# Kernel tuning notes

Measured on AMD Instinct MI355X. Metric: run time of the kernel, lower is better.

## Reference

```python
import jax, jax.numpy as jnp
import jax.scipy.linalg as jsl
import numpy as np

B, T, C = 2, 4096, 1024
HK = HV = 8           # linear_num_key_heads == linear_num_value_heads
DK = DV = 128         # linear_key_head_dim / linear_value_head_dim
CHUNK = 64
CONV_K = 4
KEY_DIM = HK * DK
VAL_DIM = HV * DV
CONV_DIM = 2 * KEY_DIM + VAL_DIM
EPS = 1e-6


def setup_inputs() -> dict:
    key = jax.random.key(0)
    ks = jax.random.split(key, 8)
    s = 0.02
    x = jax.random.normal(ks[0], (B, T, C), jnp.float32)
    W_qkvz = jax.random.normal(ks[1], (C, 2 * KEY_DIM + 2 * VAL_DIM), jnp.float32) * s
    W_ba = jax.random.normal(ks[2], (C, 2 * HV), jnp.float32) * s
    conv_w = jax.random.normal(ks[3], (CONV_DIM, 1, CONV_K), jnp.float32) * 0.3  # depthwise (O,1,K)
    dt_bias = jnp.ones((HV,), jnp.float32)
    A_log = jnp.log(jax.random.uniform(ks[4], (HV,), jnp.float32, 0.5, 8.0))
    norm_weight = jnp.ones((DV,), jnp.float32)
    W_out = jax.random.normal(ks[5], (VAL_DIM, C), jnp.float32) * s
    return {"x": x, "W_qkvz": W_qkvz, "W_ba": W_ba, "conv_w": conv_w,
            "dt_bias": dt_bias, "A_log": A_log, "norm_weight": norm_weight, "W_out": W_out}


def _l2norm(x, eps=EPS):
    return x * jax.lax.rsqrt(jnp.sum(x * x, -1, keepdims=True) + eps)


def _chunk_gated_delta_rule(q, k, v, g, beta, chunk=CHUNK):
    # q,k: (B,T,H,DK); v: (B,T,H,DV); g,beta: (B,T,H)
    q = _l2norm(q)
    k = _l2norm(k)
    tr = lambda x: jnp.swapaxes(x, 1, 2).astype(jnp.float32)  # -> (B,H,T,...)
    q, k, v, g, beta = tr(q), tr(k), tr(v), tr(g), tr(beta)
    b, h, t, dk = k.shape
    dv = v.shape[-1]
    n = t // chunk  # T divisible by chunk (pad_size == 0)
    q = q * (dk ** -0.5)
    v_beta = v * beta[..., None]
    k_beta = k * beta[..., None]
    rs = lambda x: x.reshape(b, h, n, chunk, x.shape[-1])
    q, k, v_beta, k_beta = rs(q), rs(k), rs(v_beta), rs(k_beta)
    g = jnp.cumsum(g.reshape(b, h, n, chunk), axis=-1)
    # decay_mask[..., i, j] = exp(g_i - g_j) for j <= i, else 0
    decay = jnp.tril(jnp.exp(jnp.tril(g[..., :, None] - g[..., None, :])))
    # forward substitution == unit-lower-triangular solve: (I + tri)^{-1}
    tri = jnp.tril(jnp.einsum('bhnck,bhndk->bhncd', k_beta, k) * decay, -1)
    eye = jnp.eye(chunk, dtype=jnp.float32)
    Tm = jsl.solve_triangular(eye + tri, jnp.broadcast_to(eye, tri.shape), lower=True)
    v_new = Tm @ v_beta                                   # (B,H,N,C,DV)
    k_cum = Tm @ (k_beta * jnp.exp(g)[..., None])         # (B,H,N,C,DK)
    keep_low = jnp.tril(jnp.ones((chunk, chunk), bool))

    def step(S, inp):
        q_i, k_i, v_i, kc_i, g_i, dm_i = inp              # (B,H,C,*)
        attn = jnp.where(keep_low, (q_i @ jnp.swapaxes(k_i, -1, -2)) * dm_i, 0.0)
        v_n = v_i - kc_i @ S
        out = (q_i * jnp.exp(g_i)[..., None]) @ S + attn @ v_n
        g_last = g_i[..., -1]
        S = S * jnp.exp(g_last)[..., None, None] + jnp.einsum(
            'bhck,bhcv->bhkv', k_i * jnp.exp(g_last[..., None] - g_i)[..., None], v_n)
        return S, out

    mv = lambda x: jnp.moveaxis(x, 2, 0)                  # chunk axis to front
    S0 = jnp.zeros((b, h, dk, dv), jnp.float32)
    S, outs = jax.lax.scan(step, S0, (mv(q), mv(k), mv(v_new), mv(k_cum), mv(g), mv(decay)))
    out = jnp.moveaxis(outs, 0, 2).reshape(b, h, t, dv)
    return jnp.swapaxes(out, 1, 2), S                     # (B,T,H,DV), (B,H,DK,DV)


def reference(x, W_qkvz, W_ba, conv_w, dt_bias, A_log, norm_weight, W_out):
    Bx, Tx, Cx = x.shape
    ratio = HV // HK
    qkvz = (x @ W_qkvz).reshape(Bx, Tx, HK, 2 * DK + 2 * ratio * DV)
    q, k, v, z = jnp.split(qkvz, [DK, 2 * DK, 2 * DK + ratio * DV], axis=3)
    v = v.reshape(Bx, Tx, HV, DV)
    z = z.reshape(Bx, Tx, HV, DV)
    ba = (x @ W_ba).reshape(Bx, Tx, HK, 2 * ratio)
    b_, a_ = jnp.split(ba, [ratio], axis=3)
    b_ = b_.reshape(Bx, Tx, HV)
    a_ = a_.reshape(Bx, Tx, HV)
    mixed = jnp.concatenate([q.reshape(Bx, Tx, -1), k.reshape(Bx, Tx, -1),
                             v.reshape(Bx, Tx, -1)], axis=-1)
    # causal depthwise conv1d (left pad K-1, take first T)
    xc = jnp.swapaxes(mixed, 1, 2)                        # (B, CONV_DIM, T)
    conv = jax.lax.conv_general_dilated(xc, conv_w, (1,), [(CONV_K - 1, 0)],
                                        dimension_numbers=('NCH', 'OIH', 'NCH'),
                                        feature_group_count=CONV_DIM)
    conv = jnp.swapaxes(jax.nn.silu(conv), 1, 2)          # (B,T,CONV_DIM)
    qc, kc, vc = jnp.split(conv, [KEY_DIM, 2 * KEY_DIM], axis=-1)
    qc = qc.reshape(Bx, Tx, HK, DK)
    kc = kc.reshape(Bx, Tx, HK, DK)
    vc = vc.reshape(Bx, Tx, HV, DV)
    if ratio > 1:
        qc = jnp.repeat(qc, ratio, axis=2)
        kc = jnp.repeat(kc, ratio, axis=2)
    beta = jax.nn.sigmoid(b_)
    g = -jnp.exp(A_log) * jax.nn.softplus(a_ + dt_bias)
    core, _ = _chunk_gated_delta_rule(qc, kc, vc, g, beta)
    # GatedRMSNorm over head_v_dim, gated by silu(z)
    h = core.astype(jnp.float32)
    var = jnp.mean(h * h, -1, keepdims=True)
    h = norm_weight * (h * jax.lax.rsqrt(var + EPS))
    h = h * jax.nn.silu(z.astype(jnp.float32))
    return h.reshape(Bx, Tx, VAL_DIM) @ W_out
```

## Files before the change

kernel.cpp:

```cpp
#include <hip/hip_runtime.h>
#include <cstddef>

#define Bx 2
#define Tn 4096
#define Hh 8

typedef unsigned short u16;
typedef unsigned int u32;
typedef __attribute__((ext_vector_type(8))) short short8;
typedef __attribute__((ext_vector_type(4))) float f32x4;

__device__ __forceinline__ float bf2f(u16 u) {
  u32 x = ((u32)u) << 16;
  return __uint_as_float(x);
}
__device__ __forceinline__ u16 f2bf(float f) {
  u32 x = __float_as_uint(f);
  u32 lsb = (x >> 16) & 1;
  x += 0x7fffu + lsb;
  return (u16)(x >> 16);
}
__device__ __forceinline__ u32 pack2(float a, float b) {
  return (u32)f2bf(a) | ((u32)f2bf(b) << 16);
}
__device__ __forceinline__ short8 cvt8(float4 f0, float4 f1) {
  uint4 p;
  p.x = pack2(f0.x, f0.y);
  p.y = pack2(f0.z, f0.w);
  p.z = pack2(f1.x, f1.y);
  p.w = pack2(f1.z, f1.w);
  return *(short8*)&p;
}
__device__ __forceinline__ void async16(u16* lds, const u16* g) {
  __builtin_amdgcn_global_load_lds((const __attribute__((address_space(1))) void*)g,
                                   (__attribute__((address_space(3))) void*)lds, 16, 0, 0);
}

__global__ __launch_bounds__(256) void conv_bf16(const float* __restrict__ X,
                                                 u16* __restrict__ Xb) {
  int i = (blockIdx.x * 256 + threadIdx.x) * 8;
  float4 v0 = *(const float4*)&X[i];
  float4 v1 = *(const float4*)&X[i + 4];
  uint4 pv;
  pv.x = pack2(v0.x, v0.y);
  pv.y = pack2(v0.z, v0.w);
  pv.z = pack2(v1.x, v1.y);
  pv.w = pack2(v1.z, v1.w);
  *(uint4*)&Xb[i] = pv;
}

__global__ __launch_bounds__(256) void transpose_bf16(const float* __restrict__ W,
                                                      u16* __restrict__ WT,
                                                      int K, int N) {
  __shared__ float tile[64][68];
  int nb = blockIdx.x, kb = blockIdx.y;
  int tid = threadIdx.x;
  int r = tid >> 4, c4 = (tid & 15) * 4;
#pragma unroll
  for (int p = 0; p < 4; p++) {
    int k = kb * 64 + p * 16 + r;
    float4 v = *(const float4*)&W[(size_t)k * N + nb * 64 + c4];
    tile[p * 16 + r][c4] = v.x;
    tile[p * 16 + r][c4 + 1] = v.y;
    tile[p * 16 + r][c4 + 2] = v.z;
    tile[p * 16 + r][c4 + 3] = v.w;
  }
  __syncthreads();
  int rn = tid >> 2, ck = (tid & 3) * 16;
#pragma unroll
  for (int s = 0; s < 2; s++) {
    int k0 = ck + s * 8;
    uint4 pv;
    pv.x = pack2(tile[k0 + 0][rn], tile[k0 + 1][rn]);
    pv.y = pack2(tile[k0 + 2][rn], tile[k0 + 3][rn]);
    pv.z = pack2(tile[k0 + 4][rn], tile[k0 + 5][rn]);
    pv.w = pack2(tile[k0 + 6][rn], tile[k0 + 7][rn]);
    *(uint4*)&WT[(size_t)(nb * 64 + rn) * K + kb * 64 + k0] = pv;
  }
}

__global__ __launch_bounds__(512, 1) void gemm_qkvz(const u16* __restrict__ A,
                                                    const u16* __restrict__ Bt,
                                                    u16* __restrict__ O1,
                                                    u16* __restrict__ O2) {
  const int K = 1024;
  extern __shared__ __align__(16) u16 gl[];
  int lin = blockIdx.x;
  int sl = (lin & 7) * 64 + (lin >> 3);
  int bm = sl & 31;
  int bn = sl >> 5;
  int tid = threadIdx.x;
  int wid = tid >> 6, lane = tid & 63;
  int wm = wid >> 2, wn = wid & 3;
  int m_lane = lane & 15, kgrp = lane >> 4, m7 = m_lane & 7;

  f32x4 acc[8][4];
#pragma unroll
  for (int i = 0; i < 8; i++)
#pragma unroll
    for (int j = 0; j < 4; j++) acc[i][j] = (f32x4){0.f, 0.f, 0.f, 0.f};

  int srow = lane >> 3;
  int gc8 = ((lane & 7) ^ srow) * 8;
  const u16* Ab = A + (size_t)(bm * 256 + wid * 32 + srow) * K + gc8;
  const u16* Bb = Bt + (size_t)(bn * 256 + wid * 32 + srow) * K + gc8;

#pragma unroll
  for (int i = 0; i < 4; i++) {
    async16(gl + (wid * 32 + i * 8) * 64, Ab + (size_t)(i * 8) * K);
    async16(gl + 32768 + (wid * 32 + i * 8) * 64, Bb + (size_t)(i * 8) * K);
  }
  asm volatile("s_waitcnt vmcnt(0)" ::: "memory");
  __builtin_amdgcn_s_barrier();

  for (int t = 0; t < 16; t++) {
    int p = t & 1;
    const u16* Ap = gl + p * 16384;
    const u16* Bp = gl + 32768 + p * 16384;
    if (t < 15) {
      int pn = p ^ 1;
      int kk = (t + 1) * 64;
#pragma unroll
      for (int i = 0; i < 4; i++) {
        async16(gl + pn * 16384 + (wid * 32 + i * 8) * 64, Ab + (size_t)(i * 8) * K + kk);
        async16(gl + 32768 + pn * 16384 + (wid * 32 + i * 8) * 64, Bb + (size_t)(i * 8) * K + kk);
      }
    }
    short8 bq[2][4];
#pragma unroll
    for (int ks = 0; ks < 2; ks++)
#pragma unroll
      for (int nf = 0; nf < 4; nf++)
        bq[ks][nf] = *(const short8*)&Bp[(wn * 64 + nf * 16 + m_lane) * 64 +
                                         (((ks * 4 + kgrp) ^ m7) << 3)];
#pragma unroll
    for (int mf = 0; mf < 8; mf++) {
      short8 aq0 = *(const short8*)&Ap[(wm * 128 + mf * 16 + m_lane) * 64 +
                                       ((kgrp ^ m7) << 3)];
      short8 aq1 = *(const short8*)&Ap[(wm * 128 + mf * 16 + m_lane) * 64 +
                                       (((4 + kgrp) ^ m7) << 3)];
#pragma unroll
      for (int nf = 0; nf < 4; nf++)
        acc[mf][nf] = __builtin_amdgcn_mfma_f32_16x16x32_bf16(aq0, bq[0][nf], acc[mf][nf], 0, 0, 0);
#pragma unroll
      for (int nf = 0; nf < 4; nf++)
        acc[mf][nf] = __builtin_amdgcn_mfma_f32_16x16x32_bf16(aq1, bq[1][nf], acc[mf][nf], 0, 0, 0);
    }
    if (t < 15) {
      asm volatile("s_waitcnt vmcnt(0) lgkmcnt(0)" ::: "memory");
      __builtin_amdgcn_s_barrier();
      __builtin_amdgcn_sched_barrier(0);
    }
  }

  int n0w = bn * 256 + wn * 64;
  int h = n0w >> 9, sub = (n0w >> 7) & 3;
  int cin = ((n0w & 127) & 64) + m_lane;
  u16* dst;
  size_t stride;
  if (sub < 3) { dst = O1 + (size_t)(sub * 1024 + h * 128); stride = 3072; }
  else         { dst = O2 + (size_t)(h * 128);              stride = 1024; }
  int rbase = bm * 256 + wm * 128 + kgrp * 4;
#pragma unroll
  for (int mf = 0; mf < 8; mf++)
#pragma unroll
    for (int nf = 0; nf < 4; nf++)
#pragma unroll
      for (int r = 0; r < 4; r++)
        dst[(size_t)(rbase + mf * 16 + r) * stride + cin + nf * 16] = f2bf(acc[mf][nf][r]);
}

template<int EPI>
__global__ __launch_bounds__(256) void gemm_mfma(const u16* __restrict__ A,
                                                 const u16* __restrict__ Bt,
                                                 u16* __restrict__ O1,
                                                 u16* __restrict__ O2,
                                                 float* __restrict__ O3,
                                                 int Nfull) {
  const int K = 1024;
  __shared__ u16 As[128 * 64];
  __shared__ u16 Bs[128 * 64];
  int lin = blockIdx.y * gridDim.x + blockIdx.x;
  int sl = lin >> 3;
  int cbn = gridDim.x >> 3;
  int bn = (lin & 7) * cbn + (sl % cbn);
  int bm = sl / cbn;
  int tid = threadIdx.x;
  int wave = tid >> 6, lane = tid & 63;
  int wr = wave >> 1, wc = wave & 1;

  f32x4 acc[4][4];
#pragma unroll
  for (int i = 0; i < 4; i++)
#pragma unroll
    for (int j = 0; j < 4; j++) acc[i][j] = (f32x4){0.f, 0.f, 0.f, 0.f};

  int srow = lane >> 3;
  int gc8 = ((lane & 7) ^ srow) * 8;
  const u16* Ab = A + (size_t)(bm * 128 + wave * 32 + srow) * K + gc8;
  const u16* Bb = Bt + (size_t)(bn * 128 + wave * 32 + srow) * K + gc8;
  u16* AsW = &As[(wave * 32) * 64];
  u16* BsW = &Bs[(wave * 32) * 64];

  int m_lane = lane & 15, kgrp = lane >> 4;
  int m7 = m_lane & 7;

  for (int kk = 0; kk < K; kk += 64) {
    __syncthreads();
#pragma unroll
    for (int i = 0; i < 4; i++) {
      async16(AsW + i * 512, Ab + (size_t)(i * 8) * K + kk);
      async16(BsW + i * 512, Bb + (size_t)(i * 8) * K + kk);
    }
    __syncthreads();
    short8 a[4][2], b[4][2];
#pragma unroll
    for (int t = 0; t < 4; t++)
#pragma unroll
      for (int ks = 0; ks < 2; ks++) {
        a[t][ks] = *(const short8*)&As[(wr * 64 + t * 16 + m_lane) * 64 +
                                       (((ks * 4 + kgrp) ^ m7) << 3)];
        b[t][ks] = *(const short8*)&Bs[(wc * 64 + t * 16 + m_lane) * 64 +
                                       (((ks * 4 + kgrp) ^ m7) << 3)];
      }
#pragma unroll
    for (int ks = 0; ks < 2; ks++)
#pragma unroll
      for (int i = 0; i < 4; i++)
#pragma unroll
        for (int j = 0; j < 4; j++)
          acc[i][j] = __builtin_amdgcn_mfma_f32_16x16x32_bf16(a[i][ks], b[j][ks],
                                                              acc[i][j], 0, 0, 0);
  }

  int n0 = bn * 128;
  int cbase = wc * 64 + (lane & 15);
  int rbase = bm * 128 + wr * 64 + ((lane >> 4) * 4);
  if (EPI == 1) {
    int h = n0 >> 9, sub = (n0 >> 7) & 3;
    u16* dst;
    size_t stride;
    if (sub < 3) { dst = O1 + (size_t)(sub * 1024 + h * 128); stride = 3072; }
    else         { dst = O2 + (size_t)(h * 128);              stride = 1024; }
#pragma unroll
    for (int i = 0; i < 4; i++)
#pragma unroll
      for (int j = 0; j < 4; j++)
#pragma unroll
        for (int r = 0; r < 4; r++)
          dst[(size_t)(rbase + i * 16 + r) * stride + cbase + j * 16] = f2bf(acc[i][j][r]);
  } else {
#pragma unroll
    for (int i = 0; i < 4; i++)
#pragma unroll
      for (int j = 0; j < 4; j++)
#pragma unroll
        for (int r = 0; r < 4; r++)
          O3[(size_t)(rbase + i * 16 + r) * Nfull + n0 + cbase + j * 16] = acc[i][j][r];
  }
}

__global__ __launch_bounds__(128) void ba_kernel(const float* __restrict__ x,
                                                 const float* __restrict__ Wba,
                                                 const float* __restrict__ dtb,
                                                 const float* __restrict__ Alog,
                                                 float* __restrict__ betab,
                                                 float* __restrict__ gb) {
  __shared__ float xs[1024];
  __shared__ float part[8][16];
  int row = blockIdx.x, tid = threadIdx.x;
#pragma unroll
  for (int r = 0; r < 2; r++) {
    int f4 = r * 128 + tid;
    *(float4*)&xs[f4 * 4] = *(const float4*)&x[(size_t)row * 1024 + f4 * 4];
  }
  __syncthreads();
  int col = tid & 15, seg = tid >> 4;
  float a = 0.f;
  for (int k = seg * 128; k < seg * 128 + 128; k++) a += xs[k] * Wba[k * 16 + col];
  part[seg][col] = a;
  __syncthreads();
  if (tid < 8) {
    float bval = 0.f, aval = 0.f;
#pragma unroll
    for (int q = 0; q < 8; q++) { bval += part[q][tid * 2]; aval += part[q][tid * 2 + 1]; }
    betab[(size_t)row * 8 + tid] = 1.f / (1.f + expf(-bval));
    float spin = aval + dtb[tid];
    float sp = (spin > 20.f) ? spin : log1pf(expf(spin));
    gb[(size_t)row * 8 + tid] = -expf(Alog[tid]) * sp;
  }
}

__global__ __launch_bounds__(256) void convnorm(const u16* __restrict__ mixed,
                                                const float* __restrict__ cw,
                                                const float* __restrict__ gbuf,
                                                u16* __restrict__ qn,
                                                u16* __restrict__ kn,
                                                u16* __restrict__ kdT) {
  __shared__ __align__(16) u16 sRaw[67 * 128];
  __shared__ __align__(16) u16 sO[64 * 136];
  __shared__ float red_s[256];
  __shared__ float inv_s[64];
  __shared__ float eglc_s[64];
  int n = blockIdx.x, bh = blockIdx.y, type = blockIdx.z;
  int b = bh >> 3, h = bh & 7;
  int t0 = n * 64, tid = threadIdx.x;
  int srow = tid >> 4, scol8 = (tid & 15) * 8;
  int base = type * 1024;

#pragma unroll
  for (int pass = 0; pass < 5; pass++) {
    int r = pass * 16 + srow;
    if (r < 67) {
      int t = t0 - 3 + r;
      uint4 v = make_uint4(0u, 0u, 0u, 0u);
      if (t >= 0) v = *(const uint4*)&mixed[(size_t)(b * Tn + t) * 3072 + base + h * 128 + scol8];
      *(uint4*)&sRaw[r * 128 + scol8] = v;
    }
  }
  if (type == 1 && tid < 64) {
    float gv = gbuf[(size_t)(b * Tn + t0 + tid) * 8 + h];
#pragma unroll
    for (int off = 1; off < 64; off <<= 1) {
      float o = __shfl_up(gv, off, 64);
      if (tid >= off) gv += o;
    }
    float gl = __shfl(gv, 63, 64);
    eglc_s[tid] = expf(gl - gv);
  }
  __syncthreads();

#pragma unroll
  for (int it = 0; it < 32; it++) {
    int idx = it * 256 + tid;
    int i = idx >> 7, d = idx & 127;
    int colw = (base + h * 128 + d) * 4;
    float a = 0.f;
#pragma unroll
    for (int tap = 0; tap < 4; tap++)
      a += bf2f(sRaw[(i + tap) * 128 + d]) * cw[colw + tap];
    a = a / (1.f + expf(-a));
    sO[i * 136 + d] = f2bf(a);
  }
  __syncthreads();
  {
    int i = tid >> 2, p = tid & 3;
    float ss = 0.f;
#pragma unroll
    for (int d = p * 32; d < p * 32 + 32; d += 2) {
      u32 w2 = *(const u32*)&sO[i * 136 + d];
      float a = bf2f(w2 & 0xffff), b2 = bf2f(w2 >> 16);
      ss += a * a + b2 * b2;
    }
    red_s[tid] = ss;
  }
  __syncthreads();
  if (tid < 64) {
    float inv = rsqrtf(red_s[tid * 4] + red_s[tid * 4 + 1] + red_s[tid * 4 + 2] + red_s[tid * 4 + 3] + 1e-6f);
    inv_s[tid] = (type == 0) ? inv * 0.08838834764831845f : inv;
  }
  __syncthreads();
  u16* dstRow = (type == 0 ? qn : kn) + (size_t)(bh * Tn + t0) * 128;
#pragma unroll
  for (int it = 0; it < 16; it++) {
    int idx = it * 256 + tid;
    int i = idx >> 6, d2 = (idx & 63) * 2;
    u32 w2 = *(const u32*)&sO[i * 136 + d2];
    float inv = inv_s[i];
    float q0 = bf2f(w2 & 0xffff) * inv, q1 = bf2f(w2 >> 16) * inv;
    u32 pk = pack2(q0, q1);
    if (type == 1) *(u32*)&sO[i * 136 + d2] = pk;
    *(u32*)&dstRow[(size_t)i * 128 + d2] = pk;
  }
  if (type == 1) {
    __syncthreads();
    const size_t tbase = (size_t)(bh * 64 + n) * 8192;
#pragma unroll
    for (int it = 0; it < 32; it++) {
      int idx = it * 256 + tid;
      int d = idx >> 6, i = idx & 63;
      kdT[tbase + d * 64 + i] = f2bf(bf2f(sO[i * 136 + d]) * eglc_s[i]);
    }
  }
}

__global__ __launch_bounds__(256) void prep(const u16* __restrict__ mixed,
                                            const float* __restrict__ cw,
                                            const float* __restrict__ gbuf,
                                            const float* __restrict__ betabuf,
                                            u16* qbuf,
                                            u16* kbuf,
                                            u16* __restrict__ vnT,
                                            u16* __restrict__ attn,
                                            float* __restrict__ egl) {
  __shared__ __align__(16) u16 sKn[64 * 136];
  __shared__ __align__(16) u16 sQn[64 * 136];
  __shared__ __align__(16) u16 sRawV[67 * 128];
  __shared__ float gc_s[64], egc_s[64], bet_s[64];
  float* triL = (float*)sQn;

  int n = blockIdx.x, bh = blockIdx.y;
  int b = bh >> 3, h = bh & 7;
  int t0 = n * 64;
  int tid = threadIdx.x;
  const int rowg0 = b * Tn + t0;
  const int rowh0 = bh * Tn + t0;
  const size_t tbase = (size_t)(bh * 64 + n) * 8192;

  int wv = tid >> 6, lane = tid & 63;
  int m16 = lane & 15, q8 = (lane >> 4) * 8, qr = (lane >> 4) * 4;
  int srow = tid >> 4, scol8 = (tid & 15) * 8;

#pragma unroll
  for (int it = 0; it < 4; it++) {
    int idx = it * 256 + tid;
    int i = idx >> 4, c8 = (idx & 15) * 8;
    *(uint4*)&sQn[i * 136 + c8] = *(const uint4*)&qbuf[(size_t)(rowh0 + i) * 128 + c8];
    *(uint4*)&sKn[i * 136 + c8] = *(const uint4*)&kbuf[(size_t)(rowh0 + i) * 128 + c8];
  }
#pragma unroll
  for (int pass = 0; pass < 5; pass++) {
    int r = pass * 16 + srow;
    if (r < 67) {
      int t = t0 - 3 + r;
      uint4 v = make_uint4(0u, 0u, 0u, 0u);
      if (t >= 0) v = *(const uint4*)&mixed[(size_t)(b * Tn + t) * 3072 + 2048 + h * 128 + scol8];
      *(uint4*)&sRawV[r * 128 + scol8] = v;
    }
  }
  if (tid < 64) {
    float gv = gbuf[(size_t)(rowg0 + tid) * 8 + h];
    float bv = betabuf[(size_t)(rowg0 + tid) * 8 + h];
#pragma unroll
    for (int off = 1; off < 64; off <<= 1) {
      float o = __shfl_up(gv, off, 64);
      if (tid >= off) gv += o;
    }
    float gl = __shfl(gv, 63, 64);
    gc_s[tid] = gv;
    egc_s[tid] = expf(gv);
    bet_s[tid] = bv;
    if (tid == 63) egl[bh * 64 + n] = expf(gl);
  }
  __syncthreads();

#pragma unroll
  for (int it = 0; it < 16; it++) {
    int idx = it * 256 + tid;
    int i = idx >> 6, d2 = (idx & 63) * 2;
    u32 w2 = *(const u32*)&sQn[i * 136 + d2];
    float e = egc_s[i];
    *(u32*)&qbuf[(size_t)(rowh0 + i) * 128 + d2] =
        pack2(bf2f(w2 & 0xffff) * e, bf2f(w2 >> 16) * e);
  }
  {
    short8 qa[4];
#pragma unroll
    for (int kt = 0; kt < 4; kt++)
      qa[kt] = *(const short8*)&sQn[(wv * 16 + m16) * 136 + kt * 32 + q8];
    u16* atp = attn + (size_t)(bh * 64 + n) * 4096;
#pragma unroll
    for (int jt = 0; jt < 4; jt++) {
      int j = jt * 16 + m16;
      if (jt <= wv) {
        f32x4 o = (f32x4){0.f, 0.f, 0.f, 0.f};
#pragma unroll
        for (int kt = 0; kt < 4; kt++) {
          short8 kb = *(const short8*)&sKn[(jt * 16 + m16) * 136 + kt * 32 + q8];
          o = __builtin_amdgcn_mfma_f32_16x16x32_bf16(qa[kt], kb, o, 0, 0, 0);
        }
#pragma unroll
        for (int r = 0; r < 4; r++) {
          int i = wv * 16 + qr + r;
          float val = (j <= i) ? o[r] * expf(gc_s[i] - gc_s[j]) : 0.f;
          atp[i * 64 + j] = f2bf(val);
        }
      } else {
#pragma unroll
        for (int r = 0; r < 4; r++) atp[(wv * 16 + qr + r) * 64 + j] = 0;
      }
    }
  }
  __syncthreads();
  {
    short8 ka[4];
#pragma unroll
    for (int kt = 0; kt < 4; kt++)
      ka[kt] = *(const short8*)&sKn[(wv * 16 + m16) * 136 + kt * 32 + q8];
#pragma unroll
    for (int jt = 0; jt < 4; jt++) {
      int j = jt * 16 + m16;
      if (jt <= wv) {
        f32x4 o = (f32x4){0.f, 0.f, 0.f, 0.f};
#pragma unroll
        for (int kt = 0; kt < 4; kt++) {
          short8 kb = *(const short8*)&sKn[(jt * 16 + m16) * 136 + kt * 32 + q8];
          o = __builtin_amdgcn_mfma_f32_16x16x32_bf16(ka[kt], kb, o, 0, 0, 0);
        }
#pragma unroll
        for (int r = 0; r < 4; r++) {
          int i = wv * 16 + qr + r;
          triL[i * 64 + j] = (j < i) ? bet_s[i] * expf(gc_s[i] - gc_s[j]) * o[r] : 0.f;
        }
      } else if (jt == wv + 1) {
#pragma unroll
        for (int r = 0; r < 4; r++) triL[(wv * 16 + qr + r) * 64 + j] = 0.f;
      }
    }
  }
  __syncthreads();

  {
    int mat = tid >> 7, c = tid & 127;
    float x[64];
    if (mat == 0) {
#pragma unroll
      for (int i = 0; i < 64; i++)
        x[i] = bf2f(sKn[i * 136 + c]) * bet_s[i] * egc_s[i];
    } else {
      float cwv[4];
      int colw = (2048 + h * 128 + c) * 4;
#pragma unroll
      for (int tap = 0; tap < 4; tap++) cwv[tap] = cw[colw + tap];
#pragma unroll
      for (int i = 0; i < 64; i++) {
        float a = 0.f;
#pragma unroll
        for (int tap = 0; tap < 4; tap++)
          a += bf2f(sRawV[(i + tap) * 128 + c]) * cwv[tap];
        a = a / (1.f + expf(-a));
        x[i] = a * bet_s[i];
      }
    }
#pragma unroll
    for (int i = 1; i < 64; i++) {
      float s0 = 0.f, s1 = 0.f, s2 = 0.f, s3 = 0.f;
#pragma unroll
      for (int l4 = 0; l4 < (i + 3) / 4; l4++) {
        float4 t4 = *(float4*)&triL[i * 64 + l4 * 4];
        s0 += t4.x * x[l4 * 4 + 0];
        s1 += t4.y * x[l4 * 4 + 1];
        s2 += t4.z * x[l4 * 4 + 2];
        s3 += t4.w * x[l4 * 4 + 3];
      }
      x[i] = x[i] - ((s0 + s1) + (s2 + s3));
    }
    if (mat == 0) {
#pragma unroll
      for (int i = 0; i < 64; i++) kbuf[(size_t)(rowh0 + i) * 128 + c] = f2bf(-x[i]);
    } else {
#pragma unroll
      for (int i = 0; i < 64; i += 2)
        *(u32*)&vnT[tbase + c * 64 + i] = pack2(x[i], x[i + 1]);
    }
  }
}

__device__ __forceinline__ void stage_quarter(int w, u16* ldsb,
                                              const u16* __restrict__ qgc,
                                              const u16* __restrict__ kcc,
                                              const u16* __restrict__ ktc,
                                              const u16* __restrict__ atc,
                                              const u16* __restrict__ vtc,
                                              int lane) {
  int l8 = lane * 8;
  if (w == 0) {
#pragma unroll
    for (int i = 0; i < 16; i++) {
      int p = i * 512 + l8;
      async16(ldsb + 8192 + i * 512, kcc + (p ^ ((((p >> 7) & 15)) << 3)));
    }
  } else if (w == 1) {
#pragma unroll
    for (int i = 0; i < 16; i++) {
      int p = i * 512 + l8;
      async16(ldsb + 16384 + i * 512, ktc + (p ^ ((((p >> 6) & 7)) << 3)));
    }
  } else if (w == 2) {
#pragma unroll
    for (int i = 0; i < 16; i++) {
      int p = i * 512 + l8;
      async16(ldsb + i * 512, qgc + (p ^ ((((p >> 7) & 15)) << 3)));
    }
  } else {
#pragma unroll
    for (int i = 0; i < 8; i++) {
      int p = i * 512 + l8;
      async16(ldsb + 24576 + i * 512, atc + (p ^ ((((p >> 6) & 7)) << 3)));
    }
#pragma unroll
    for (int i = 0; i < 2; i++) {
      int p = i * 512 + l8;
      async16(ldsb + 28672 + i * 512, vtc + (p ^ ((((p >> 6) & 7)) << 3)));
    }
  }
}

__global__ __launch_bounds__(256, 1) void scan_mfma(const u16* __restrict__ qg,
                                                    const u16* __restrict__ kdT,
                                                    const u16* __restrict__ vnT,
                                                    const u16* __restrict__ kcum,
                                                    const u16* __restrict__ attn,
                                                    const float* __restrict__ egl,
                                                    float* __restrict__ core) {
  extern __shared__ __align__(16) u16 dyn[];
  __shared__ __align__(16) u16 STb[16 * 128];
  __shared__ __align__(16) u16 VNb[16 * 64];
  int blk = blockIdx.x;
  int bh = blk & 15, tile = blk >> 4;
  int dv0 = tile * 16;
  int b = bh >> 3, h = bh & 7;
  int tid = threadIdx.x;
  int w = tid >> 6, lane = tid & 63;
  int q = lane >> 4, col = lane & 15;
  int c7 = col & 7;
  int qh = q >> 1, ql = q & 1;

  for (int r = tid; r < 16 * 128 / 2; r += 256) ((u32*)STb)[r] = 0u;
  float egAll = egl[bh * 64 + lane];

  f32x4 st0 = (f32x4){0.f, 0.f, 0.f, 0.f};
  f32x4 st1 = (f32x4){0.f, 0.f, 0.f, 0.f};

  const u16* qg_base = qg + (size_t)bh * Tn * 128;
  const u16* kc_base = kcum + (size_t)bh * Tn * 128;
  const u16* kt_base = kdT + (size_t)bh * 64 * 8192;
  const u16* at_base = attn + (size_t)bh * 64 * 4096;
  const u16* vt_base = vnT + (size_t)bh * 64 * 8192 + dv0 * 64;

  stage_quarter(w, dyn, qg_base, kc_base, kt_base, at_base, vt_base, lane);
  asm volatile("s_waitcnt vmcnt(0)" ::: "memory");
  __syncthreads();

  for (int n = 0; n < 64; n++) {
    u16* buf = dyn + (n & 1) * 29696;

    short8 kcf[4], qgf[4], ktf[4], atf[2], sb[4];
    uint2 vtf;
#pragma unroll
    for (int kt = 0; kt < 4; kt++) {
      kcf[kt] = *(const short8*)&buf[8192 + (w * 16 + col) * 128 + (((kt * 4 + q) ^ col) << 3)];
      qgf[kt] = *(const short8*)&buf[(w * 16 + col) * 128 + (((kt * 4 + q) ^ col) << 3)];
      sb[kt] = *(const short8*)&STb[col * 128 + (((kt * 4 + q) ^ col) << 3)];
    }
#pragma unroll
    for (int kt2 = 0; kt2 < 2; kt2++) {
      atf[kt2] = *(const short8*)&buf[24576 + (w * 16 + col) * 64 + (((kt2 * 4 + q) ^ c7) << 3)];
#pragma unroll
      for (int t = 0; t < 2; t++)
        ktf[t * 2 + kt2] = *(const short8*)&buf[16384 + ((w * 2 + t) * 16 + col) * 64 +
                                                (((kt2 * 4 + q) ^ c7) << 3)];
    }
    vtf = *(const uint2*)&buf[28672 + col * 64 + (((w * 2 + qh) ^ c7) << 3) + ql * 4];

    if (n < 63) {
      stage_quarter(w, dyn + ((n + 1) & 1) * 29696,
                    qg_base + (size_t)(n + 1) * 8192,
                    kc_base + (size_t)(n + 1) * 8192,
                    kt_base + (size_t)(n + 1) * 8192,
                    at_base + (size_t)(n + 1) * 4096,
                    vt_base + (size_t)(n + 1) * 8192, lane);
    }
    float eg = __shfl(egAll, n, 64);

    {
      f32x4 a0;
      a0[0] = bf2f(vtf.x & 0xffff); a0[1] = bf2f(vtf.x >> 16);
      a0[2] = bf2f(vtf.y & 0xffff); a0[3] = bf2f(vtf.y >> 16);
#pragma unroll
      for (int kt = 0; kt < 4; kt++)
        a0 = __builtin_amdgcn_mfma_f32_16x16x32_bf16(kcf[kt], sb[kt], a0, 0, 0, 0);
      uint2 pk;
      pk.x = pack2(a0[0], a0[1]);
      pk.y = pack2(a0[2], a0[3]);
      *(uint2*)&VNb[col * 64 + (((w * 2 + qh) ^ c7) << 3) + ql * 4] = pk;
    }
    asm volatile("s_waitcnt lgkmcnt(0)" ::: "memory");
    __builtin_amdgcn_s_barrier();
    __builtin_amdgcn_sched_barrier(0);

    short8 vb[2];
#pragma unroll
    for (int kt2 = 0; kt2 < 2; kt2++)
      vb[kt2] = *(const short8*)&VNb[col * 64 + (((kt2 * 4 + q) ^ c7) << 3)];

    {
      f32x4 s0;
      s0[0] = st0[0] * eg; s0[1] = st0[1] * eg; s0[2] = st0[2] * eg; s0[3] = st0[3] * eg;
      s0 = __builtin_amdgcn_mfma_f32_16x16x32_bf16(ktf[0], vb[0], s0, 0, 0, 0);
      s0 = __builtin_amdgcn_mfma_f32_16x16x32_bf16(ktf[1], vb[1], s0, 0, 0, 0);
      st0 = s0;
      uint2 pk;
      pk.x = pack2(s0[0], s0[1]);
      pk.y = pack2(s0[2], s0[3]);
      *(uint2*)&STb[col * 128 + ((((w * 2 + 0) * 2 + qh) ^ col) << 3) + ql * 4] = pk;
    }
    {
      f32x4 s1;
      s1[0] = st1[0] * eg; s1[1] = st1[1] * eg; s1[2] = st1[2] * eg; s1[3] = st1[3] * eg;
      s1 = __builtin_amdgcn_mfma_f32_16x16x32_bf16(ktf[2], vb[0], s1, 0, 0, 0);
      s1 = __builtin_amdgcn_mfma_f32_16x16x32_bf16(ktf[3], vb[1], s1, 0, 0, 0);
      st1 = s1;
      uint2 pk;
      pk.x = pack2(s1[0], s1[1]);
      pk.y = pack2(s1[2], s1[3]);
      *(uint2*)&STb[col * 128 + ((((w * 2 + 1) * 2 + qh) ^ col) << 3) + ql * 4] = pk;
    }

    {
      f32x4 o = (f32x4){0.f, 0.f, 0.f, 0.f};
#pragma unroll
      for (int kt = 0; kt < 4; kt++)
        o = __builtin_amdgcn_mfma_f32_16x16x32_bf16(qgf[kt], sb[kt], o, 0, 0, 0);
#pragma unroll
      for (int kt2 = 0; kt2 < 2; kt2++)
        o = __builtin_amdgcn_mfma_f32_16x16x32_bf16(atf[kt2], vb[kt2], o, 0, 0, 0);
      size_t rowb = (size_t)(b * Tn) + n * 64 + w * 16 + q * 4;
#pragma unroll
      for (int r2 = 0; r2 < 4; r2++)
        core[(rowb + r2) * 1024 + h * 128 + dv0 + col] = o[r2];
    }

    asm volatile("s_waitcnt vmcnt(4) lgkmcnt(0)" ::: "memory");
    __builtin_amdgcn_s_barrier();
    __builtin_amdgcn_sched_barrier(0);
  }
}

__global__ __launch_bounds__(256) void gnorm(const float* __restrict__ core,
                                             const u16* __restrict__ z,
                                             const float* __restrict__ nw,
                                             u16* __restrict__ coreb) {
  __shared__ float red[256];
  __shared__ float rstd[8];
  int row = blockIdx.x, tid = threadIdx.x;
  float4 c4 = *(const float4*)&core[(size_t)row * 1024 + tid * 4];
  uint2 zl = *(const uint2*)&z[(size_t)row * 1024 + tid * 4];
  float4 z4;
  z4.x = bf2f(zl.x & 0xffff); z4.y = bf2f(zl.x >> 16);
  z4.z = bf2f(zl.y & 0xffff); z4.w = bf2f(zl.y >> 16);
  red[tid] = c4.x * c4.x + c4.y * c4.y + c4.z * c4.z + c4.w * c4.w;
  __syncthreads();
  if (tid < 8) {
    float s = 0.f;
    for (int t2 = tid * 32; t2 < tid * 32 + 32; t2++) s += red[t2];
    rstd[tid] = rsqrtf(s * (1.f / 128.f) + 1e-6f);
  }
  __syncthreads();
  float rs = rstd[tid >> 5];
  int d0 = (tid * 4) & 127;
  float4 w4 = *(const float4*)&nw[d0];
  float4 o;
  o.x = c4.x * rs * w4.x * (z4.x / (1.f + expf(-z4.x)));
  o.y = c4.y * rs * w4.y * (z4.y / (1.f + expf(-z4.y)));
  o.z = c4.z * rs * w4.z * (z4.z / (1.f + expf(-z4.z)));
  o.w = c4.w * rs * w4.w * (z4.w / (1.f + expf(-z4.w)));
  uint2 pv;
  pv.x = pack2(o.x, o.y);
  pv.y = pack2(o.z, o.w);
  *(uint2*)&coreb[(size_t)row * 1024 + tid * 4] = pv;
}

extern "C" void kernel_launch(void* const* d_in, const int* in_sizes, int n_in,
                              void* d_out, int out_size, void* d_ws, size_t ws_size,
                              hipStream_t stream) {
  const float* x     = (const float*)d_in[0];
  const float* Wqkvz = (const float*)d_in[1];
  const float* Wba   = (const float*)d_in[2];
  const float* convw = (const float*)d_in[3];
  const float* dtb   = (const float*)d_in[4];
  const float* Alog  = (const float*)d_in[5];
  const float* nw    = (const float*)d_in[6];
  const float* Wout  = (const float*)d_in[7];
  float* out = (float*)d_out;

  char* w = (char*)d_ws;
  u16*   mixed = (u16*)w;
  float* core  = (float*)w;
  u16*   coreb = (u16*)(w + 33554432);
  u16*   zb    = (u16*)(w + 50331648);
  float* betab = (float*)(w + 67108864);
  float* gb    = (float*)(w + 67371008);
  u16*   qgB   = (u16*)(w + 67633152);
  u16*   xb    = (u16*)(w + 67633152);
  u16*   kdTB  = (u16*)(w + 84410368);
  u16*   WqT   = (u16*)(w + 84410368);
  u16*   vnTB  = (u16*)(w + 101187584);
  u16*   kcB   = (u16*)(w + 117964800);
  u16*   WoT   = (u16*)(w + 117964800);
  u16*   atB   = (u16*)(w + 134742016);
  float* eglB  = (float*)(w + 143130624);

  static bool attr_set = false;
  if (!attr_set) {
    hipFuncSetAttribute(reinterpret_cast<const void*>(scan_mfma),
                        hipFuncAttributeMaxDynamicSharedMemorySize, 118784);
    hipFuncSetAttribute(reinterpret_cast<const void*>(gemm_qkvz),
                        hipFuncAttributeMaxDynamicSharedMemorySize, 131072);
    attr_set = true;
  }

  conv_bf16<<<dim3(4096), 256, 0, stream>>>(x, xb);
  transpose_bf16<<<dim3(64, 16), 256, 0, stream>>>(Wqkvz, WqT, 1024, 4096);
  gemm_qkvz<<<dim3(512), 512, 131072, stream>>>(xb, WqT, mixed, zb);
  ba_kernel<<<dim3(8192), 128, 0, stream>>>(x, Wba, dtb, Alog, betab, gb);
  convnorm<<<dim3(64, 16, 2), 256, 0, stream>>>(mixed, convw, gb, qgB, kcB, kdTB);
  prep<<<dim3(64, 16), 256, 0, stream>>>(mixed, convw, gb, betab, qgB, kcB, vnTB, atB, eglB);
  scan_mfma<<<dim3(128), 256, 118784, stream>>>(qgB, kdTB, vnTB, kcB, atB, eglB, core);
  transpose_bf16<<<dim3(16, 16), 256, 0, stream>>>(Wout, WoT, 1024, 1024);
  gnorm<<<dim3(8192), 256, 0, stream>>>(core, zb, nw, coreb);
  gemm_mfma<0><<<dim3(8, 64), 256, 0, stream>>>(coreb, WoT, nullptr, nullptr, out, 1024);
}
```

Baseline: 396.9 us.

## Load scan fragments straight from global into register double buffers, dropping LDS staging

The chunked scan kernel used to stage each chunk's q/k/kT/attn/v tiles through a double-buffered dynamic LDS region with async copies, then read MFMA fragments back out of LDS. Now each wave loads its MFMA fragments directly from global memory into registers, one chunk ahead, using two register fragment sets that alternate in a loop unrolled by two. This removes the LDS round-trip, the dynamic shared memory allocation and the vmcnt wait at the per-chunk barrier. In exchange it uses more registers and relies on one iteration of prefetch being enough to cover global-load latency, with the compiler inserting the waits before first use.

```diff
diff --git a/kernel.cpp b/kernel.cpp
--- a/kernel.cpp
+++ b/kernel.cpp
@@ -556,44 +556,113 @@
   }
 }
 
-__device__ __forceinline__ void stage_quarter(int w, u16* ldsb,
-                                              const u16* __restrict__ qgc,
-                                              const u16* __restrict__ kcc,
-                                              const u16* __restrict__ ktc,
-                                              const u16* __restrict__ atc,
-                                              const u16* __restrict__ vtc,
-                                              int lane) {
-  int l8 = lane * 8;
-  if (w == 0) {
-#pragma unroll
-    for (int i = 0; i < 16; i++) {
-      int p = i * 512 + l8;
-      async16(ldsb + 8192 + i * 512, kcc + (p ^ ((((p >> 7) & 15)) << 3)));
-    }
-  } else if (w == 1) {
-#pragma unroll
-    for (int i = 0; i < 16; i++) {
-      int p = i * 512 + l8;
-      async16(ldsb + 16384 + i * 512, ktc + (p ^ ((((p >> 6) & 7)) << 3)));
-    }
-  } else if (w == 2) {
-#pragma unroll
-    for (int i = 0; i < 16; i++) {
-      int p = i * 512 + l8;
-      async16(ldsb + i * 512, qgc + (p ^ ((((p >> 7) & 15)) << 3)));
-    }
-  } else {
-#pragma unroll
-    for (int i = 0; i < 8; i++) {
-      int p = i * 512 + l8;
-      async16(ldsb + 24576 + i * 512, atc + (p ^ ((((p >> 6) & 7)) << 3)));
-    }
-#pragma unroll
-    for (int i = 0; i < 2; i++) {
-      int p = i * 512 + l8;
-      async16(ldsb + 28672 + i * 512, vtc + (p ^ ((((p >> 6) & 7)) << 3)));
-    }
-  }
+struct ScanFrag {
+  short8 kcf[4], qgf[4], ktf[4], atf[2];
+  uint2 vtf;
+};
+
+__device__ __forceinline__ void scan_load(ScanFrag& f,
+                                          const u16* __restrict__ qg_n,
+                                          const u16* __restrict__ kc_n,
+                                          const u16* __restrict__ kt_n,
+                                          const u16* __restrict__ at_n,
+                                          const u16* __restrict__ vt_n,
+                                          int w, int col, int q) {
+#pragma unroll
+  for (int kt = 0; kt < 4; kt++) {
+    f.kcf[kt] = *(const short8*)&kc_n[(w * 16 + col) * 128 + kt * 32 + q * 8];
+    f.qgf[kt] = *(const short8*)&qg_n[(w * 16 + col) * 128 + kt * 32 + q * 8];
+  }
+#pragma unroll
+  for (int kt2 = 0; kt2 < 2; kt2++) {
+    f.atf[kt2] = *(const short8*)&at_n[(w * 16 + col) * 64 + kt2 * 32 + q * 8];
+#pragma unroll
+    for (int t = 0; t < 2; t++)
+      f.ktf[t * 2 + kt2] = *(const short8*)&kt_n[((w * 2 + t) * 16 + col) * 64 + kt2 * 32 + q * 8];
+  }
+  f.vtf = *(const uint2*)&vt_n[col * 64 + w * 16 + q * 4];
+}
+
+__device__ __forceinline__ void scan_iter(
+    const ScanFrag& f, ScanFrag& fn, bool pf, int n,
+    const u16* __restrict__ qg_base, const u16* __restrict__ kc_base,
+    const u16* __restrict__ kt_base, const u16* __restrict__ at_base,
+    const u16* __restrict__ vt_base,
+    u16* STb, u16* VNb, f32x4& st0, f32x4& st1, float egAll,
+    int w, int col, int q, int c7, int qh, int ql,
+    float* __restrict__ core, int b, int h, int dv0) {
+  short8 sb[4];
+#pragma unroll
+  for (int kt = 0; kt < 4; kt++)
+    sb[kt] = *(const short8*)&STb[col * 128 + (((kt * 4 + q) ^ col) << 3)];
+  if (pf)
+    scan_load(fn, qg_base + (size_t)(n + 1) * 8192, kc_base + (size_t)(n + 1) * 8192,
+              kt_base + (size_t)(n + 1) * 8192, at_base + (size_t)(n + 1) * 4096,
+              vt_base + (size_t)(n + 1) * 8192, w, col, q);
+  __builtin_amdgcn_sched_barrier(0);
+  float eg = __shfl(egAll, n, 64);
+
+  {
+    f32x4 a0;
+    a0[0] = bf2f(f.vtf.x & 0xffff); a0[1] = bf2f(f.vtf.x >> 16);
+    a0[2] = bf2f(f.vtf.y & 0xffff); a0[3] = bf2f(f.vtf.y >> 16);
+#pragma unroll
+    for (int kt = 0; kt < 4; kt++)
+      a0 = __builtin_amdgcn_mfma_f32_16x16x32_bf16(f.kcf[kt], sb[kt], a0, 0, 0, 0);
+    uint2 pk;
+    pk.x = pack2(a0[0], a0[1]);
+    pk.y = pack2(a0[2], a0[3]);
+    *(uint2*)&VNb[col * 64 + (((w * 2 + qh) ^ c7) << 3) + ql * 4] = pk;
+  }
+  asm volatile("s_waitcnt lgkmcnt(0)" ::: "memory");
+  __builtin_amdgcn_s_barrier();
+  __builtin_amdgcn_sched_barrier(0);
+
+  short8 vb[2];
+#pragma unroll
+  for (int kt2 = 0; kt2 < 2; kt2++)
+    vb[kt2] = *(const short8*)&VNb[col * 64 + (((kt2 * 4 + q) ^ c7) << 3)];
+
+  {
+    f32x4 s0;
+    s0[0] = st0[0] * eg; s0[1] = st0[1] * eg; s0[2] = st0[2] * eg; s0[3] = st0[3] * eg;
+    s0 = __builtin_amdgcn_mfma_f32_16x16x32_bf16(f.ktf[0], vb[0], s0, 0, 0, 0);
+    s0 = __builtin_amdgcn_mfma_f32_16x16x32_bf16(f.ktf[1], vb[1], s0, 0, 0, 0);
+    st0 = s0;
+    uint2 pk;
+    pk.x = pack2(s0[0], s0[1]);
+    pk.y = pack2(s0[2], s0[3]);
+    *(uint2*)&STb[col * 128 + ((((w * 2 + 0) * 2 + qh) ^ col) << 3) + ql * 4] = pk;
+  }
+  {
+    f32x4 s1;
+    s1[0] = st1[0] * eg; s1[1] = st1[1] * eg; s1[2] = st1[2] * eg; s1[3] = st1[3] * eg;
+    s1 = __builtin_amdgcn_mfma_f32_16x16x32_bf16(f.ktf[2], vb[0], s1, 0, 0, 0);
+    s1 = __builtin_amdgcn_mfma_f32_16x16x32_bf16(f.ktf[3], vb[1], s1, 0, 0, 0);
+    st1 = s1;
+    uint2 pk;
+    pk.x = pack2(s1[0], s1[1]);
+    pk.y = pack2(s1[2], s1[3]);
+    *(uint2*)&STb[col * 128 + ((((w * 2 + 1) * 2 + qh) ^ col) << 3) + ql * 4] = pk;
+  }
+
+  {
+    f32x4 o = (f32x4){0.f, 0.f, 0.f, 0.f};
+#pragma unroll
+    for (int kt = 0; kt < 4; kt++)
+      o = __builtin_amdgcn_mfma_f32_16x16x32_bf16(f.qgf[kt], sb[kt], o, 0, 0, 0);
+#pragma unroll
+    for (int kt2 = 0; kt2 < 2; kt2++)
+      o = __builtin_amdgcn_mfma_f32_16x16x32_bf16(f.atf[kt2], vb[kt2], o, 0, 0, 0);
+    size_t rowb = (size_t)(b * Tn) + n * 64 + w * 16 + q * 4;
+#pragma unroll
+    for (int r2 = 0; r2 < 4; r2++)
+      core[(rowb + r2) * 1024 + h * 128 + dv0 + col] = o[r2];
+  }
+
+  asm volatile("s_waitcnt lgkmcnt(0)" ::: "memory");
+  __builtin_amdgcn_s_barrier();
+  __builtin_amdgcn_sched_barrier(0);
 }
 
 __global__ __launch_bounds__(256, 1) void scan_mfma(const u16* __restrict__ qg,
@@ -603,7 +672,6 @@
                                                     const u16* __restrict__ attn,
                                                     const float* __restrict__ egl,
                                                     float* __restrict__ core) {
-  extern __shared__ __align__(16) u16 dyn[];
   __shared__ __align__(16) u16 STb[16 * 128];
   __shared__ __align__(16) u16 VNb[16 * 64];
   int blk = blockIdx.x;
@@ -628,102 +696,15 @@
   const u16* at_base = attn + (size_t)bh * 64 * 4096;
   const u16* vt_base = vnT + (size_t)bh * 64 * 8192 + dv0 * 64;
 
-  stage_quarter(w, dyn, qg_base, kc_base, kt_base, at_base, vt_base, lane);
-  asm volatile("s_waitcnt vmcnt(0)" ::: "memory");
-  __syncthreads();
-
-  for (int n = 0; n < 64; n++) {
-    u16* buf = dyn + (n & 1) * 29696;
-
-    short8 kcf[4], qgf[4], ktf[4], atf[2], sb[4];
-    uint2 vtf;
-#pragma unroll
-    for (int kt = 0; kt < 4; kt++) {
-      kcf[kt] = *(const short8*)&buf[8192 + (w * 16 + col) * 128 + (((kt * 4 + q) ^ col) << 3)];
-      qgf[kt] = *(const short8*)&buf[(w * 16 + col) * 128 + (((kt * 4 + q) ^ col) << 3)];
-      sb[kt] = *(const short8*)&STb[col * 128 + (((kt * 4 + q) ^ col) << 3)];
-    }
-#pragma unroll
-    for (int kt2 = 0; kt2 < 2; kt2++) {
-      atf[kt2] = *(const short8*)&buf[24576 + (w * 16 + col) * 64 + (((kt2 * 4 + q) ^ c7) << 3)];
-#pragma unroll
-      for (int t = 0; t < 2; t++)
-        ktf[t * 2 + kt2] = *(const short8*)&buf[16384 + ((w * 2 + t) * 16 + col) * 64 +
-                                                (((kt2 * 4 + q) ^ c7) << 3)];
-    }
-    vtf = *(const uint2*)&buf[28672 + col * 64 + (((w * 2 + qh) ^ c7) << 3) + ql * 4];
-
-    if (n < 63) {
-      stage_quarter(w, dyn + ((n + 1) & 1) * 29696,
-                    qg_base + (size_t)(n + 1) * 8192,
-                    kc_base + (size_t)(n + 1) * 8192,
-                    kt_base + (size_t)(n + 1) * 8192,
-                    at_base + (size_t)(n + 1) * 4096,
-                    vt_base + (size_t)(n + 1) * 8192, lane);
-    }
-    float eg = __shfl(egAll, n, 64);
-
-    {
-      f32x4 a0;
-      a0[0] = bf2f(vtf.x & 0xffff); a0[1] = bf2f(vtf.x >> 16);
-      a0[2] = bf2f(vtf.y & 0xffff); a0[3] = bf2f(vtf.y >> 16);
-#pragma unroll
-      for (int kt = 0; kt < 4; kt++)
-        a0 = __builtin_amdgcn_mfma_f32_16x16x32_bf16(kcf[kt], sb[kt], a0, 0, 0, 0);
-      uint2 pk;
-      pk.x = pack2(a0[0], a0[1]);
-      pk.y = pack2(a0[2], a0[3]);
-      *(uint2*)&VNb[col * 64 + (((w * 2 + qh) ^ c7) << 3) + ql * 4] = pk;
-    }
-    asm volatile("s_waitcnt lgkmcnt(0)" ::: "memory");
-    __builtin_amdgcn_s_barrier();
-    __builtin_amdgcn_sched_barrier(0);
-
-    short8 vb[2];
-#pragma unroll
-    for (int kt2 = 0; kt2 < 2; kt2++)
-      vb[kt2] = *(const short8*)&VNb[col * 64 + (((kt2 * 4 + q) ^ c7) << 3)];
-
-    {
-      f32x4 s0;
-      s0[0] = st0[0] * eg; s0[1] = st0[1] * eg; s0[2] = st0[2] * eg; s0[3] = st0[3] * eg;
-      s0 = __builtin_amdgcn_mfma_f32_16x16x32_bf16(ktf[0], vb[0], s0, 0, 0, 0);
-      s0 = __builtin_amdgcn_mfma_f32_16x16x32_bf16(ktf[1], vb[1], s0, 0, 0, 0);
-      st0 = s0;
-      uint2 pk;
-      pk.x = pack2(s0[0], s0[1]);
-      pk.y = pack2(s0[2], s0[3]);
-      *(uint2*)&STb[col * 128 + ((((w * 2 + 0) * 2 + qh) ^ col) << 3) + ql * 4] = pk;
-    }
-    {
-      f32x4 s1;
-      s1[0] = st1[0] * eg; s1[1] = st1[1] * eg; s1[2] = st1[2] * eg; s1[3] = st1[3] * eg;
-      s1 = __builtin_amdgcn_mfma_f32_16x16x32_bf16(ktf[2], vb[0], s1, 0, 0, 0);
-      s1 = __builtin_amdgcn_mfma_f32_16x16x32_bf16(ktf[3], vb[1], s1, 0, 0, 0);
-      st1 = s1;
-      uint2 pk;
-      pk.x = pack2(s1[0], s1[1]);
-      pk.y = pack2(s1[2], s1[3]);
-      *(uint2*)&STb[col * 128 + ((((w * 2 + 1) * 2 + qh) ^ col) << 3) + ql * 4] = pk;
-    }
-
-    {
-      f32x4 o = (f32x4){0.f, 0.f, 0.f, 0.f};
-#pragma unroll
-      for (int kt = 0; kt < 4; kt++)
-        o = __builtin_amdgcn_mfma_f32_16x16x32_bf16(qgf[kt], sb[kt], o, 0, 0, 0);
-#pragma unroll
-      for (int kt2 = 0; kt2 < 2; kt2++)
-        o = __builtin_amdgcn_mfma_f32_16x16x32_bf16(atf[kt2], vb[kt2], o, 0, 0, 0);
-      size_t rowb = (size_t)(b * Tn) + n * 64 + w * 16 + q * 4;
-#pragma unroll
-      for (int r2 = 0; r2 < 4; r2++)
-        core[(rowb + r2) * 1024 + h * 128 + dv0 + col] = o[r2];
-    }
-
-    asm volatile("s_waitcnt vmcnt(4) lgkmcnt(0)" ::: "memory");
-    __builtin_amdgcn_s_barrier();
-    __builtin_amdgcn_sched_barrier(0);
+  ScanFrag fA, fB;
+  scan_load(fA, qg_base, kc_base, kt_base, at_base, vt_base, w, col, q);
+  __syncthreads();
+
+  for (int n = 0; n < 64; n += 2) {
+    scan_iter(fA, fB, true, n, qg_base, kc_base, kt_base, at_base, vt_base,
+              STb, VNb, st0, st1, egAll, w, col, q, c7, qh, ql, core, b, h, dv0);
+    scan_iter(fB, fA, n + 2 < 64, n + 1, qg_base, kc_base, kt_base, at_base, vt_base,
+              STb, VNb, st0, st1, egAll, w, col, q, c7, qh, ql, core, b, h, dv0);
   }
 }
 
@@ -793,8 +774,6 @@
 
   static bool attr_set = false;
   if (!attr_set) {
-    hipFuncSetAttribute(reinterpret_cast<const void*>(scan_mfma),
-                        hipFuncAttributeMaxDynamicSharedMemorySize, 118784);
     hipFuncSetAttribute(reinterpret_cast<const void*>(gemm_qkvz),
                         hipFuncAttributeMaxDynamicSharedMemorySize, 131072);
     attr_set = true;
@@ -806,7 +785,7 @@
   ba_kernel<<<dim3(8192), 128, 0, stream>>>(x, Wba, dtb, Alog, betab, gb);
   convnorm<<<dim3(64, 16, 2), 256, 0, stream>>>(mixed, convw, gb, qgB, kcB, kdTB);
   prep<<<dim3(64, 16), 256, 0, stream>>>(mixed, convw, gb, betab, qgB, kcB, vnTB, atB, eglB);
-  scan_mfma<<<dim3(128), 256, 118784, stream>>>(qgB, kdTB, vnTB, kcB, atB, eglB, core);
+  scan_mfma<<<dim3(128), 256, 0, stream>>>(qgB, kdTB, vnTB, kcB, atB, eglB, core);
   transpose_bf16<<<dim3(16, 16), 256, 0, stream>>>(Wout, WoT, 1024, 1024);
   gnorm<<<dim3(8192), 256, 0, stream>>>(core, zb, nw, coreb);
   gemm_mfma<0><<<dim3(8, 64), 256, 0, stream>>>(coreb, WoT, nullptr, nullptr, out, 1024);
```

After: 444.4 us. +12.0%, slower.
